# Kernel tuning notes

Hardware: AMD Instinct MI355X
Metric: run time of the kernel (lower is better)

Reference implementation:

```python
import jax, jax.numpy as jnp
import numpy as np

EMBED = 128
HEADS = 16
N = 10000
E = 160000
NEG_SLOPE = 0.2


def setup_inputs() -> dict:
    key = jax.random.key(0)
    ks = jax.random.split(key, 12)
    s = 0.05
    return {
        "x": jax.random.normal(ks[0], (N, EMBED), jnp.float32),
        "edge_index": jax.random.randint(ks[1], (2, E), 0, N, jnp.int64),
        # gat1: in=EMBED, out=EMBED, heads=16, concat
        "W1": jax.random.normal(ks[2], (EMBED, HEADS * EMBED), jnp.float32) * s,
        "a_src1": jax.random.normal(ks[3], (HEADS, EMBED), jnp.float32) * s,
        "a_dst1": jax.random.normal(ks[4], (HEADS, EMBED), jnp.float32) * s,
        "b1": jnp.zeros((HEADS * EMBED,), jnp.float32),
        # gat2: in=HEADS*EMBED, out=EMBED, heads=1, no concat
        "W2": jax.random.normal(ks[5], (HEADS * EMBED, EMBED), jnp.float32) * s,
        "a_src2": jax.random.normal(ks[6], (1, EMBED), jnp.float32) * s,
        "a_dst2": jax.random.normal(ks[7], (1, EMBED), jnp.float32) * s,
        "b2": jnp.zeros((EMBED,), jnp.float32),
        # classifier
        "Wc": jax.random.normal(ks[8], (EMBED, 1), jnp.float32) * s,
        "bc": jnp.zeros((1,), jnp.float32),
    }


def _gat_layer(x, src, dst, W, a_src, a_dst, b, heads, out_ch, n_nodes):
    # node projection: [N, H, C]
    h = (x @ W).reshape(n_nodes, heads, out_ch)
    # per-node attention logits [N, H]
    al_s = jnp.einsum('nhc,hc->nh', h, a_src)
    al_d = jnp.einsum('nhc,hc->nh', h, a_dst)
    # per-edge logits [E, H]
    e = jax.nn.leaky_relu(al_s[src] + al_d[dst], NEG_SLOPE)
    # segment softmax over incoming edges of each dst node
    m = jax.ops.segment_max(e, dst, num_segments=n_nodes)
    ex = jnp.exp(e - m[dst])
    z = jax.ops.segment_sum(ex, dst, num_segments=n_nodes)
    alpha = ex / (z[dst] + 1e-16)
    # weighted scatter-aggregate [N, H, C]
    msg = h[src] * alpha[:, :, None]
    out = jax.ops.segment_sum(msg, dst, num_segments=n_nodes)
    return out.reshape(n_nodes, heads * out_ch) + b


def reference(x, edge_index, W1, a_src1, a_dst1, b1, W2, a_src2, a_dst2, b2, Wc, bc):
    n_nodes = x.shape[0]
    # PyG GATConv default: add self loops
    loop = jnp.arange(n_nodes, dtype=edge_index.dtype)
    src = jnp.concatenate([edge_index[0], loop])
    dst = jnp.concatenate([edge_index[1], loop])
    h = _gat_layer(x, src, dst, W1, a_src1, a_dst1, b1, HEADS, EMBED, n_nodes)
    h = jax.nn.elu(h)
    h = _gat_layer(h, src, dst, W2, a_src2, a_dst2, b2, 1, EMBED, n_nodes)
    return h @ Wc + bc  # [N, 1]
```

## Files before the change

### kernel.cpp

```cpp
#include <hip/hip_runtime.h>
#include <hip/hip_bf16.h>

#define EMBED 128
#define HEADS 16
#define NEG 0.2f

typedef __attribute__((ext_vector_type(8))) short short8;
typedef __attribute__((ext_vector_type(4))) float floatx4;

static __device__ __forceinline__ float leaky(float x) { return x > 0.f ? x : NEG * x; }

static __device__ __forceinline__ short f2bf_bits(float f) {
  __hip_bfloat16 h = __float2bfloat16(f);
  union { __hip_bfloat16 b; short s; } u;
  u.b = h;
  return u.s;
}


__global__ void k_hist(const int* __restrict__ ei, int E, int N, int* __restrict__ deg) {
  int i = blockIdx.x * blockDim.x + threadIdx.x;
  int Et = E + N;
  if (i >= Et) return;
  int d = (i < E) ? ei[E + i] : (i - E);
  atomicAdd(&deg[d], 1);
}

__global__ __launch_bounds__(256) void k_scan1(const int* __restrict__ deg,
                                               int* __restrict__ excl,
                                               int* __restrict__ bsum, int n) {
  __shared__ int s[256];
  int i = blockIdx.x * 256 + threadIdx.x;
  int v = (i < n) ? deg[i] : 0;
  s[threadIdx.x] = v;
  __syncthreads();
  for (int d = 1; d < 256; d <<= 1) {
    int add = ((int)threadIdx.x >= d) ? s[threadIdx.x - d] : 0;
    __syncthreads();
    s[threadIdx.x] += add;
    __syncthreads();
  }
  if (i < n) excl[i] = s[threadIdx.x] - v;
  if (threadIdx.x == 255) bsum[blockIdx.x] = s[255];
}

__global__ void k_scan2(int* __restrict__ bsum, int nb) {
  if (threadIdx.x == 0 && blockIdx.x == 0) {
    int acc = 0;
    for (int i = 0; i < nb; ++i) { int v = bsum[i]; bsum[i] = acc; acc += v; }
  }
}

__global__ __launch_bounds__(256) void k_scan3(const int* __restrict__ deg,
                                               const int* __restrict__ excl,
                                               const int* __restrict__ bsum,
                                               int* __restrict__ row_ptr,
                                               int* __restrict__ cursor, int n) {
  int i = blockIdx.x * 256 + threadIdx.x;
  if (i < n) {
    int r = excl[i] + bsum[blockIdx.x];
    row_ptr[i] = r;
    cursor[i] = r;
    if (i == n - 1) row_ptr[n] = r + deg[i];
  }
}

__global__ void k_scatter(const int* __restrict__ ei, int E, int N,
                          int* __restrict__ cursor, int* __restrict__ csr_src) {
  int i = blockIdx.x * blockDim.x + threadIdx.x;
  int Et = E + N;
  if (i >= Et) return;
  int s = (i < E) ? ei[i] : (i - E);
  int d = (i < E) ? ei[E + i] : (i - E);
  int pos = atomicAdd(&cursor[d], 1);
  csr_src[pos] = s;
}


__global__ __launch_bounds__(256) void k_prepAll(const float* __restrict__ W1,
                                                 const float* __restrict__ a_src1,
                                                 const float* __restrict__ a_dst1,
                                                 const float* __restrict__ W2,
                                                 const float* __restrict__ a_src2,
                                                 const float* __restrict__ a_dst2,
                                                 const float* __restrict__ Wc,
                                                 const float* __restrict__ b2,
                                                 const float* __restrict__ bc,
                                                 float* __restrict__ wsAll,
                                                 float* __restrict__ uvec,
                                                 float* __restrict__ cconst) {
  int gid = blockIdx.x * 256 + threadIdx.x;
  if (gid < 4096) {
    int sel = gid >> 11;
    int id = gid & 2047;
    int h = id >> 7, k = id & 127;
    const float* av = sel ? a_dst1 : a_src1;
    float sum = 0.f;
    const float* wrow = W1 + (size_t)k * 2048 + h * 128;
    const float* arow = av + h * 128;
#pragma unroll 4
    for (int c = 0; c < 128; ++c) sum += wrow[c] * arow[c];
    wsAll[gid] = sum;
  } else if (gid < 10240) {
    int g = gid - 4096;
    int sel = g >> 11;
    int k = g & 2047;
    const float* v = sel == 0 ? Wc : (sel == 1 ? a_src2 : a_dst2);
    const float* wrow = W2 + (size_t)k * 128;
    float s = 0.f;
#pragma unroll 4
    for (int j = 0; j < 128; ++j) s += wrow[j] * v[j];
    uvec[g] = s;
  } else if (gid == 10240) {
    float s = 0.f;
    for (int j = 0; j < 128; ++j) s += b2[j] * Wc[j];
    *cconst = s + bc[0];
  }
}


__global__ __launch_bounds__(256) void k_prep2aT(const float* __restrict__ W1,
                                                 short* __restrict__ hi,
                                                 short* __restrict__ lo) {
  __shared__ float tile[64][65];
  int h = blockIdx.x;
  int c0 = blockIdx.y * 64;
  int j0 = blockIdx.z * 64;
  int t = threadIdx.x;
#pragma unroll
  for (int i = 0; i < 4; ++i) {
    int idx4 = i * 256 + t;
    int c = idx4 >> 4, j4 = idx4 & 15;
    float4 v = *(const float4*)&W1[(size_t)(c0 + c) * 2048 + h * 128 + j0 + j4 * 4];
    tile[c][j4 * 4 + 0] = v.x;
    tile[c][j4 * 4 + 1] = v.y;
    tile[c][j4 * 4 + 2] = v.z;
    tile[c][j4 * 4 + 3] = v.w;
  }
  __syncthreads();
#pragma unroll
  for (int i = 0; i < 4; ++i) {
    int idx = i * 256 + t;
    int j = idx >> 4, c4 = idx & 15;
    unsigned short vh[4], vl[4];
#pragma unroll
    for (int ii = 0; ii < 4; ++ii) {
      float wv = tile[c4 * 4 + ii][j];
      short hb = f2bf_bits(wv);
      float hf = __uint_as_float(((unsigned int)(unsigned short)hb) << 16);
      vh[ii] = (unsigned short)hb;
      vl[ii] = (unsigned short)f2bf_bits(wv - hf);
    }
    size_t o = (size_t)h * 16384 + (size_t)(j0 + j) * 128 + c0 + c4 * 4;
    *(ushort4*)&hi[o] = make_ushort4(vh[0], vh[1], vh[2], vh[3]);
    *(ushort4*)&lo[o] = make_ushort4(vl[0], vl[1], vl[2], vl[3]);
  }
}


__global__ __launch_bounds__(256) void k_al1v2(const float* __restrict__ x,
                                               const float* __restrict__ wsAll,
                                               float* __restrict__ als,
                                               float* __restrict__ ald, int N) {
  __shared__ float wss[128][16], wsd[128][16];
  int tid = threadIdx.x;
  for (int i = tid; i < 2048; i += 256) {
    int h = i >> 7, c = i & 127;
    wss[c][h] = wsAll[i];
    wsd[c][h] = wsAll[2048 + i];
  }
  __syncthreads();
  int gid = blockIdx.x * 256 + tid;
  int n = gid >> 4, h = gid & 15;
  if (n >= N) return;
  const float4* xp = (const float4*)(x + (size_t)n * 128);
  float ps = 0.f, pd = 0.f;
#pragma unroll 8
  for (int c4 = 0; c4 < 32; ++c4) {
    float4 xv = xp[c4];
    int c = c4 * 4;
    ps += xv.x * wss[c][h] + xv.y * wss[c + 1][h] + xv.z * wss[c + 2][h] + xv.w * wss[c + 3][h];
    pd += xv.x * wsd[c][h] + xv.y * wsd[c + 1][h] + xv.z * wsd[c + 2][h] + xv.w * wsd[c + 3][h];
  }
  als[gid] = ps;
  ald[gid] = pd;
}


__global__ __launch_bounds__(256) void k_attn1h(const float* __restrict__ x,
                                                const float* __restrict__ als,
                                                const float* __restrict__ ald,
                                                const int* __restrict__ row_ptr,
                                                const int* __restrict__ csr,
                                                __hip_bfloat16* __restrict__ xaggb,
                                                int N) {
  __shared__ float accsh[2][64][37];

  int tid = threadIdx.x;
  int w = tid >> 6, lane = tid & 63;
  int slot = w >> 1, half = w & 1;
  int d = blockIdx.x * 2 + slot;
  bool active = d < N;

  int e0 = 0, deg = 0;
  if (active) {
    e0 = row_ptr[d];
    deg = row_ptr[d + 1] - e0;
  }

  int g = lane >> 4, c8 = lane & 15;
  float4 aldh4;
  if (active) aldh4 = *(const float4*)&ald[(size_t)d * 16 + g * 4];
  else aldh4 = make_float4(0.f, 0.f, 0.f, 0.f);

  float acc[4][8];
  float zacc[4] = {0.f, 0.f, 0.f, 0.f};
#pragma unroll
  for (int hh = 0; hh < 4; ++hh)
#pragma unroll
    for (int i = 0; i < 8; ++i) acc[hh][i] = 0.f;

  if (active) {
    const float* xc = x + c8 * 8;
    for (int e = half; e < deg; e += 2) {
      int s = csr[e0 + e];
      float4 alv = *(const float4*)&als[(size_t)s * 16 + g * 4];
      const float4* xp = (const float4*)(xc + (size_t)s * 128);
      float4 xa = xp[0], xb = xp[1];
      float ev0 = __expf(leaky(alv.x + aldh4.x));
      float ev1 = __expf(leaky(alv.y + aldh4.y));
      float ev2 = __expf(leaky(alv.z + aldh4.z));
      float ev3 = __expf(leaky(alv.w + aldh4.w));
      zacc[0] += ev0; zacc[1] += ev1; zacc[2] += ev2; zacc[3] += ev3;
      acc[0][0] += ev0 * xa.x; acc[0][1] += ev0 * xa.y; acc[0][2] += ev0 * xa.z; acc[0][3] += ev0 * xa.w;
      acc[0][4] += ev0 * xb.x; acc[0][5] += ev0 * xb.y; acc[0][6] += ev0 * xb.z; acc[0][7] += ev0 * xb.w;
      acc[1][0] += ev1 * xa.x; acc[1][1] += ev1 * xa.y; acc[1][2] += ev1 * xa.z; acc[1][3] += ev1 * xa.w;
      acc[1][4] += ev1 * xb.x; acc[1][5] += ev1 * xb.y; acc[1][6] += ev1 * xb.z; acc[1][7] += ev1 * xb.w;
      acc[2][0] += ev2 * xa.x; acc[2][1] += ev2 * xa.y; acc[2][2] += ev2 * xa.z; acc[2][3] += ev2 * xa.w;
      acc[2][4] += ev2 * xb.x; acc[2][5] += ev2 * xb.y; acc[2][6] += ev2 * xb.z; acc[2][7] += ev2 * xb.w;
      acc[3][0] += ev3 * xa.x; acc[3][1] += ev3 * xa.y; acc[3][2] += ev3 * xa.z; acc[3][3] += ev3 * xa.w;
      acc[3][4] += ev3 * xb.x; acc[3][5] += ev3 * xb.y; acc[3][6] += ev3 * xb.z; acc[3][7] += ev3 * xb.w;
    }
  }

  if (half == 1) {
#pragma unroll
    for (int hh = 0; hh < 4; ++hh) {
#pragma unroll
      for (int i = 0; i < 8; ++i)
        accsh[slot][lane][hh * 8 + i] = acc[hh][i];
      accsh[slot][lane][32 + hh] = zacc[hh];
    }
  }
  __syncthreads();
  if (half == 0 && active) {
#pragma unroll
    for (int hh = 0; hh < 4; ++hh) {
      int h = g * 4 + hh;
      float z = zacc[hh] + accsh[slot][lane][32 + hh];
      float iz = 1.f / (z + 1e-16f);
      __hip_bfloat16 t[8];
#pragma unroll
      for (int i = 0; i < 8; ++i) {
        float v = (acc[hh][i] + accsh[slot][lane][hh * 8 + i]) * iz;
        t[i] = __float2bfloat16(v);
      }
      *(uint4*)(xaggb + (size_t)h * N * 128 + (size_t)d * 128 + c8 * 8) = *(uint4*)t;
    }
  }
}


__global__ __launch_bounds__(256, 2) void k_fused(const __hip_bfloat16* __restrict__ xaggb,
                                                  const short* __restrict__ w1t_hi,
                                                  const short* __restrict__ w1t_lo,
                                                  const float* __restrict__ b1,
                                                  const float* __restrict__ uvec,
                                                  float* __restrict__ partH,
                                                  int N) {
  __shared__ float sh[512];
  __shared__ __align__(16) char Bh[32768];
  __shared__ __align__(16) char Bl[32768];
  int tid = threadIdx.x;
  int h = blockIdx.y;
  int n0 = blockIdx.x * 256;

  for (int i = tid; i < 512; i += 256) {
    int arr = i >> 7, jj = i & 127;
    sh[i] = (arr == 0) ? b1[h * 128 + jj] : uvec[(arr - 1) * 2048 + h * 128 + jj];
  }
  const char* gbh = (const char*)(w1t_hi + (size_t)h * 16384);
  const char* gbl = (const char*)(w1t_lo + (size_t)h * 16384);
#pragma unroll
  for (int i = 0; i < 8; ++i) {
    int ci = i * 256 + tid;
    int row = ci >> 4, kc = ci & 15;
    int po = row * 256 + ((kc ^ (row & 15)) << 4);
    *(uint4*)(Bh + po) = *(const uint4*)(gbh + ci * 16);
    *(uint4*)(Bl + po) = *(const uint4*)(gbl + ci * 16);
  }

  int w = tid >> 6, lane = tid & 63;
  int quad = lane >> 4, l15 = lane & 15;
  int nw = n0 + w * 64;

  const char* abase = (const char*)xaggb + (size_t)h * N * 256;
  short8 a[4][4];
#pragma unroll
  for (int nt = 0; nt < 4; ++nt) {
    int node = nw + nt * 16 + l15;
    if (node >= N) node = N - 1;
    const char* rowp = abase + (size_t)node * 256 + quad * 16;
#pragma unroll
    for (int ks = 0; ks < 4; ++ks)
      a[nt][ks] = *(const short8*)(rowp + ks * 64);
  }
  __syncthreads();

  floatx4 acc[4][8];
#pragma unroll
  for (int jt = 0; jt < 8; ++jt) {
    floatx4 bb = *(const floatx4*)&sh[jt * 16 + quad * 4];
#pragma unroll
    for (int nt = 0; nt < 4; ++nt) acc[nt][jt] = bb;
  }

  for (int ks = 0; ks < 4; ++ks) {
    int xo = (((ks * 4 + quad) ^ l15) << 4);
#pragma unroll
    for (int jt = 0; jt < 8; ++jt) {
      int po = (jt * 16 + l15) * 256 + xo;
      short8 wh = *(const short8*)(Bh + po);
      short8 wl = *(const short8*)(Bl + po);
#pragma unroll
      for (int nt = 0; nt < 4; ++nt) {
        acc[nt][jt] = __builtin_amdgcn_mfma_f32_16x16x32_bf16(wh, a[nt][ks], acc[nt][jt], 0, 0, 0);
        acc[nt][jt] = __builtin_amdgcn_mfma_f32_16x16x32_bf16(wl, a[nt][ks], acc[nt][jt], 0, 0, 0);
      }
    }
  }

  float pc[4] = {0.f, 0.f, 0.f, 0.f};
  float ps[4] = {0.f, 0.f, 0.f, 0.f};
  float pd[4] = {0.f, 0.f, 0.f, 0.f};
#pragma unroll
  for (int jt = 0; jt < 8; ++jt) {
    floatx4 uc = *(const floatx4*)&sh[128 + jt * 16 + quad * 4];
    floatx4 us = *(const floatx4*)&sh[256 + jt * 16 + quad * 4];
    floatx4 ud = *(const floatx4*)&sh[384 + jt * 16 + quad * 4];
#pragma unroll
    for (int nt = 0; nt < 4; ++nt) {
#pragma unroll
      for (int r = 0; r < 4; ++r) {
        float v = acc[nt][jt][r];
        float e = v > 0.f ? v : (__expf(v) - 1.f);
        pc[nt] += e * uc[r];
        ps[nt] += e * us[r];
        pd[nt] += e * ud[r];
      }
    }
  }
  float* pcH = partH + (size_t)h * N;
  float* psH = partH + (size_t)(16 + h) * N;
  float* pdH = partH + (size_t)(32 + h) * N;
#pragma unroll
  for (int nt = 0; nt < 4; ++nt) {
    float c = pc[nt], s = ps[nt], dd = pd[nt];
    c += __shfl_xor(c, 16); c += __shfl_xor(c, 32);
    s += __shfl_xor(s, 16); s += __shfl_xor(s, 32);
    dd += __shfl_xor(dd, 16); dd += __shfl_xor(dd, 32);
    int node = nw + nt * 16 + l15;
    if (quad == 0 && node < N) {
      pcH[node] = c;
      psH[node] = s;
      pdH[node] = dd;
    }
  }
}


__global__ __launch_bounds__(256) void k_redparts(const float* __restrict__ partH,
                                                  float* __restrict__ partc,
                                                  float* __restrict__ parts,
                                                  float* __restrict__ partd, int N) {
  int n = blockIdx.x * 256 + threadIdx.x;
  if (n >= N) return;
  float c = 0.f, s = 0.f, d = 0.f;
#pragma unroll
  for (int h = 0; h < 16; ++h) {
    c += partH[(size_t)h * N + n];
    s += partH[(size_t)(16 + h) * N + n];
    d += partH[(size_t)(32 + h) * N + n];
  }
  partc[n] = c;
  parts[n] = s;
  partd[n] = d;
}


__global__ __launch_bounds__(256) void k_attn2s(const float* __restrict__ partc,
                                                const float* __restrict__ parts,
                                                const float* __restrict__ partd,
                                                const int* __restrict__ row_ptr,
                                                const int* __restrict__ csr,
                                                const float* __restrict__ cconst,
                                                float* __restrict__ out, int N) {
  int w = threadIdx.x >> 6, lane = threadIdx.x & 63;
  int d = blockIdx.x * 4 + w;
  if (d >= N) return;
  int e0 = row_ptr[d], deg = row_ptr[d + 1] - e0;
  float aldd = partd[d];
  float z = 0.f, num = 0.f;
  for (int e = lane; e < deg; e += 64) {
    int s = csr[e0 + e];
    float v = __expf(leaky(parts[s] + aldd));
    z += v;
    num += v * partc[s];
  }
#pragma unroll
  for (int off = 32; off; off >>= 1) {
    z += __shfl_xor(z, off);
    num += __shfl_xor(num, off);
  }
  if (lane == 0) out[d] = num / (z + 1e-16f) + cconst[0];
}


extern "C" void kernel_launch(void* const* d_in, const int* in_sizes, int n_in,
                              void* d_out, int out_size, void* d_ws, size_t ws_size,
                              hipStream_t stream) {
  const float* x      = (const float*)d_in[0];
  const int*   ei     = (const int*)d_in[1];
  const float* W1     = (const float*)d_in[2];
  const float* a_src1 = (const float*)d_in[3];
  const float* a_dst1 = (const float*)d_in[4];
  const float* b1     = (const float*)d_in[5];
  const float* W2     = (const float*)d_in[6];
  const float* a_src2 = (const float*)d_in[7];
  const float* a_dst2 = (const float*)d_in[8];
  const float* b2     = (const float*)d_in[9];
  const float* Wc     = (const float*)d_in[10];
  const float* bc     = (const float*)d_in[11];

  int N = in_sizes[0] / EMBED;
  int E = in_sizes[1] / 2;
  int Et = E + N;
  int nScanB = (N + 255) / 256;

  char* ws = (char*)d_ws;
  size_t off = 0;
  auto alloc = [&](size_t bytes) -> void* {
    void* p = ws + off;
    off += (bytes + 255) & ~(size_t)255;
    return p;
  };
  __hip_bfloat16* xaggb = (__hip_bfloat16*)alloc((size_t)N * 2048 * 2 + 65536);
  short* w1t_hi = (short*)alloc((size_t)262144 * 2);
  short* w1t_lo = (short*)alloc((size_t)262144 * 2);
  float* wsAll  = (float*)alloc(4096 * 4);
  float* uvec   = (float*)alloc(6144 * 4);
  float* cconst = (float*)alloc(256);
  float* als1   = (float*)alloc((size_t)N * 16 * 4);
  float* ald1   = (float*)alloc((size_t)N * 16 * 4);
  float* partH  = (float*)alloc((size_t)48 * N * 4);
  float* part   = (float*)alloc((size_t)3 * N * 4);
  float* partc  = part;
  float* parts  = part + N;
  float* partd  = part + 2 * N;
  int* deg      = (int*)alloc((size_t)N * 4);
  int* excl     = (int*)alloc((size_t)N * 4);
  int* bsum     = (int*)alloc((size_t)(nScanB + 1) * 4);
  int* row_ptr  = (int*)alloc((size_t)(N + 1) * 4);
  int* cursor   = (int*)alloc((size_t)N * 4);
  int* csr      = (int*)alloc((size_t)Et * 4);

  hipMemsetAsync(deg, 0, (size_t)N * 4, stream);

  k_hist<<<(Et + 255) / 256, 256, 0, stream>>>(ei, E, N, deg);
  k_scan1<<<nScanB, 256, 0, stream>>>(deg, excl, bsum, N);
  k_scan2<<<1, 64, 0, stream>>>(bsum, nScanB);
  k_scan3<<<nScanB, 256, 0, stream>>>(deg, excl, bsum, row_ptr, cursor, N);
  k_scatter<<<(Et + 255) / 256, 256, 0, stream>>>(ei, E, N, cursor, csr);

  k_prepAll<<<41, 256, 0, stream>>>(W1, a_src1, a_dst1, W2, a_src2, a_dst2, Wc, b2, bc,
                                    wsAll, uvec, cconst);
  k_prep2aT<<<dim3(16, 2, 2), 256, 0, stream>>>(W1, w1t_hi, w1t_lo);

  k_al1v2<<<(N * 16 + 255) / 256, 256, 0, stream>>>(x, wsAll, als1, ald1, N);
  k_attn1h<<<(N + 1) / 2, 256, 0, stream>>>(x, als1, ald1, row_ptr, csr, xaggb, N);

  k_fused<<<dim3((N + 255) / 256, 16), 256, 0, stream>>>(xaggb, w1t_hi, w1t_lo, b1, uvec,
                                                         partH, N);
  k_redparts<<<(N + 255) / 256, 256, 0, stream>>>(partH, partc, parts, partd, N);
  k_attn2s<<<(N + 3) / 4, 256, 0, stream>>>(partc, parts, partd, row_ptr, csr, cconst,
                                            (float*)d_out, N);
}
```

Measured before the change: 189.9 us.

## Merge prep kernels, single-block scan, atomic head reduction, prefetch attention gathers

Folds the two weight-prep kernels and the buffer zeroing into one launch, and replaces the three-kernel scan with a single-block wave-shuffle scan. The separate per-head reduction kernel is removed: the fused GEMM kernel now accumulates its per-head partials straight into the final vectors with float atomics. The layer-1 attention loop caches CSR indices in registers and software-prefetches the next edge's gathers. Layer-2 attention uses 16 lanes per node instead of 64. The aim is fewer launches and better latency hiding, at the cost of atomic contention and summation order that is no longer deterministic.

New measurement: 183.5 us. 3.4% less time.

```diff
diff --git a/kernel.cpp b/kernel.cpp
--- a/kernel.cpp
+++ b/kernel.cpp
@@ -26,43 +26,40 @@
   atomicAdd(&deg[d], 1);
 }
 
-__global__ __launch_bounds__(256) void k_scan1(const int* __restrict__ deg,
-                                               int* __restrict__ excl,
-                                               int* __restrict__ bsum, int n) {
-  __shared__ int s[256];
-  int i = blockIdx.x * 256 + threadIdx.x;
-  int v = (i < n) ? deg[i] : 0;
-  s[threadIdx.x] = v;
-  __syncthreads();
-  for (int d = 1; d < 256; d <<= 1) {
-    int add = ((int)threadIdx.x >= d) ? s[threadIdx.x - d] : 0;
+__global__ __launch_bounds__(1024) void k_scan(const int* __restrict__ deg,
+                                               int* __restrict__ row_ptr,
+                                               int* __restrict__ cursor, int N) {
+  __shared__ int wsum[16];
+  int tid = threadIdx.x;
+  int lane = tid & 63, w = tid >> 6;
+  int base = 0;
+  for (int c0 = 0; c0 < N; c0 += 1024) {
+    int i = c0 + tid;
+    int v = (i < N) ? deg[i] : 0;
+    int s = v;
+#pragma unroll
+    for (int dd = 1; dd < 64; dd <<= 1) {
+      int t = __shfl_up(s, dd);
+      if (lane >= dd) s += t;
+    }
+    if (lane == 63) wsum[w] = s;
     __syncthreads();
-    s[threadIdx.x] += add;
+    int carry = 0, ctot = 0;
+#pragma unroll
+    for (int k = 0; k < 16; ++k) {
+      int t = wsum[k];
+      ctot += t;
+      if (k < w) carry += t;
+    }
+    int excl = base + carry + s - v;
+    if (i < N) {
+      row_ptr[i] = excl;
+      cursor[i] = excl;
+    }
+    base += ctot;
     __syncthreads();
   }
-  if (i < n) excl[i] = s[threadIdx.x] - v;
-  if (threadIdx.x == 255) bsum[blockIdx.x] = s[255];
-}
-
-__global__ void k_scan2(int* __restrict__ bsum, int nb) {
-  if (threadIdx.x == 0 && blockIdx.x == 0) {
-    int acc = 0;
-    for (int i = 0; i < nb; ++i) { int v = bsum[i]; bsum[i] = acc; acc += v; }
-  }
-}
-
-__global__ __launch_bounds__(256) void k_scan3(const int* __restrict__ deg,
-                                               const int* __restrict__ excl,
-                                               const int* __restrict__ bsum,
-                                               int* __restrict__ row_ptr,
-                                               int* __restrict__ cursor, int n) {
-  int i = blockIdx.x * 256 + threadIdx.x;
-  if (i < n) {
-    int r = excl[i] + bsum[blockIdx.x];
-    row_ptr[i] = r;
-    cursor[i] = r;
-    if (i == n - 1) row_ptr[n] = r + deg[i];
-  }
+  if (tid == 0) row_ptr[N] = base;
 }
 
 __global__ void k_scatter(const int* __restrict__ ei, int E, int N,
@@ -77,19 +74,61 @@
 }
 
 
-__global__ __launch_bounds__(256) void k_prepAll(const float* __restrict__ W1,
-                                                 const float* __restrict__ a_src1,
-                                                 const float* __restrict__ a_dst1,
-                                                 const float* __restrict__ W2,
-                                                 const float* __restrict__ a_src2,
-                                                 const float* __restrict__ a_dst2,
-                                                 const float* __restrict__ Wc,
-                                                 const float* __restrict__ b2,
-                                                 const float* __restrict__ bc,
-                                                 float* __restrict__ wsAll,
-                                                 float* __restrict__ uvec,
-                                                 float* __restrict__ cconst) {
-  int gid = blockIdx.x * 256 + threadIdx.x;
+__global__ __launch_bounds__(256) void k_prep(const float* __restrict__ W1,
+                                              const float* __restrict__ a_src1,
+                                              const float* __restrict__ a_dst1,
+                                              const float* __restrict__ W2,
+                                              const float* __restrict__ a_src2,
+                                              const float* __restrict__ a_dst2,
+                                              const float* __restrict__ Wc,
+                                              const float* __restrict__ b2,
+                                              const float* __restrict__ bc,
+                                              float* __restrict__ wsAll,
+                                              float* __restrict__ uvec,
+                                              float* __restrict__ cconst,
+                                              short* __restrict__ hi,
+                                              short* __restrict__ lo,
+                                              float* __restrict__ part,
+                                              int* __restrict__ deg,
+                                              int N) {
+  __shared__ float tile[64][65];
+  if (blockIdx.x < 64) {
+    int b = blockIdx.x;
+    int h = b & 15;
+    int c0 = ((b >> 4) & 1) * 64;
+    int j0 = ((b >> 5) & 1) * 64;
+    int t = threadIdx.x;
+#pragma unroll
+    for (int i = 0; i < 4; ++i) {
+      int idx4 = i * 256 + t;
+      int c = idx4 >> 4, j4 = idx4 & 15;
+      float4 v = *(const float4*)&W1[(size_t)(c0 + c) * 2048 + h * 128 + j0 + j4 * 4];
+      tile[c][j4 * 4 + 0] = v.x;
+      tile[c][j4 * 4 + 1] = v.y;
+      tile[c][j4 * 4 + 2] = v.z;
+      tile[c][j4 * 4 + 3] = v.w;
+    }
+    __syncthreads();
+#pragma unroll
+    for (int i = 0; i < 4; ++i) {
+      int idx = i * 256 + t;
+      int j = idx >> 4, c4 = idx & 15;
+      unsigned short vh[4], vl[4];
+#pragma unroll
+      for (int ii = 0; ii < 4; ++ii) {
+        float wv = tile[c4 * 4 + ii][j];
+        short hb = f2bf_bits(wv);
+        float hf = __uint_as_float(((unsigned int)(unsigned short)hb) << 16);
+        vh[ii] = (unsigned short)hb;
+        vl[ii] = (unsigned short)f2bf_bits(wv - hf);
+      }
+      size_t o = (size_t)h * 16384 + (size_t)(j0 + j) * 128 + c0 + c4 * 4;
+      *(ushort4*)&hi[o] = make_ushort4(vh[0], vh[1], vh[2], vh[3]);
+      *(ushort4*)&lo[o] = make_ushort4(vl[0], vl[1], vl[2], vl[3]);
+    }
+    return;
+  }
+  int gid = (blockIdx.x - 64) * 256 + threadIdx.x;
   if (gid < 4096) {
     int sel = gid >> 11;
     int id = gid & 2047;
@@ -115,45 +154,10 @@
     float s = 0.f;
     for (int j = 0; j < 128; ++j) s += b2[j] * Wc[j];
     *cconst = s + bc[0];
-  }
-}
-
-
-__global__ __launch_bounds__(256) void k_prep2aT(const float* __restrict__ W1,
-                                                 short* __restrict__ hi,
-                                                 short* __restrict__ lo) {
-  __shared__ float tile[64][65];
-  int h = blockIdx.x;
-  int c0 = blockIdx.y * 64;
-  int j0 = blockIdx.z * 64;
-  int t = threadIdx.x;
-#pragma unroll
-  for (int i = 0; i < 4; ++i) {
-    int idx4 = i * 256 + t;
-    int c = idx4 >> 4, j4 = idx4 & 15;
-    float4 v = *(const float4*)&W1[(size_t)(c0 + c) * 2048 + h * 128 + j0 + j4 * 4];
-    tile[c][j4 * 4 + 0] = v.x;
-    tile[c][j4 * 4 + 1] = v.y;
-    tile[c][j4 * 4 + 2] = v.z;
-    tile[c][j4 * 4 + 3] = v.w;
-  }
-  __syncthreads();
-#pragma unroll
-  for (int i = 0; i < 4; ++i) {
-    int idx = i * 256 + t;
-    int j = idx >> 4, c4 = idx & 15;
-    unsigned short vh[4], vl[4];
-#pragma unroll
-    for (int ii = 0; ii < 4; ++ii) {
-      float wv = tile[c4 * 4 + ii][j];
-      short hb = f2bf_bits(wv);
-      float hf = __uint_as_float(((unsigned int)(unsigned short)hb) << 16);
-      vh[ii] = (unsigned short)hb;
-      vl[ii] = (unsigned short)f2bf_bits(wv - hf);
-    }
-    size_t o = (size_t)h * 16384 + (size_t)(j0 + j) * 128 + c0 + c4 * 4;
-    *(ushort4*)&hi[o] = make_ushort4(vh[0], vh[1], vh[2], vh[3]);
-    *(ushort4*)&lo[o] = make_ushort4(vl[0], vl[1], vl[2], vl[3]);
+  } else if (gid >= 10496) {
+    int z = gid - 10496;
+    if (z < 3 * N) part[z] = 0.f;
+    else if (z < 4 * N) deg[z - 3 * N] = 0;
   }
 }
 
@@ -209,9 +213,8 @@
   }
 
   int g = lane >> 4, c8 = lane & 15;
-  float4 aldh4;
+  float4 aldh4 = make_float4(0.f, 0.f, 0.f, 0.f);
   if (active) aldh4 = *(const float4*)&ald[(size_t)d * 16 + g * 4];
-  else aldh4 = make_float4(0.f, 0.f, 0.f, 0.f);
 
   float acc[4][8];
   float zacc[4] = {0.f, 0.f, 0.f, 0.f};
@@ -221,25 +224,53 @@
     for (int i = 0; i < 8; ++i) acc[hh][i] = 0.f;
 
   if (active) {
+    int sreg = 0;
+    if (lane < deg) sreg = csr[e0 + lane];
     const float* xc = x + c8 * 8;
-    for (int e = half; e < deg; e += 2) {
-      int s = csr[e0 + e];
-      float4 alv = *(const float4*)&als[(size_t)s * 16 + g * 4];
-      const float4* xp = (const float4*)(xc + (size_t)s * 128);
-      float4 xa = xp[0], xb = xp[1];
-      float ev0 = __expf(leaky(alv.x + aldh4.x));
-      float ev1 = __expf(leaky(alv.y + aldh4.y));
-      float ev2 = __expf(leaky(alv.z + aldh4.z));
-      float ev3 = __expf(leaky(alv.w + aldh4.w));
+
+    int e = half;
+    bool have = e < deg;
+    int sC = 0;
+    float4 alC = make_float4(0.f, 0.f, 0.f, 0.f);
+    float4 xaC = alC, xbC = alC;
+    if (have) {
+      sC = (e < 64) ? __shfl(sreg, e) : csr[e0 + e];
+      alC = *(const float4*)&als[(size_t)sC * 16 + g * 4];
+      const float4* xp = (const float4*)(xc + (size_t)sC * 128);
+      xaC = xp[0];
+      xbC = xp[1];
+    }
+    while (have) {
+      int e2 = e + 2;
+      bool have2 = e2 < deg;
+      int sN = 0;
+      float4 alN = alC, xaN = xaC, xbN = xbC;
+      if (have2) {
+        sN = (e2 < 64) ? __shfl(sreg, e2) : csr[e0 + e2];
+        alN = *(const float4*)&als[(size_t)sN * 16 + g * 4];
+        const float4* xp2 = (const float4*)(xc + (size_t)sN * 128);
+        xaN = xp2[0];
+        xbN = xp2[1];
+      }
+      float ev0 = __expf(leaky(alC.x + aldh4.x));
+      float ev1 = __expf(leaky(alC.y + aldh4.y));
+      float ev2 = __expf(leaky(alC.z + aldh4.z));
+      float ev3 = __expf(leaky(alC.w + aldh4.w));
       zacc[0] += ev0; zacc[1] += ev1; zacc[2] += ev2; zacc[3] += ev3;
-      acc[0][0] += ev0 * xa.x; acc[0][1] += ev0 * xa.y; acc[0][2] += ev0 * xa.z; acc[0][3] += ev0 * xa.w;
-      acc[0][4] += ev0 * xb.x; acc[0][5] += ev0 * xb.y; acc[0][6] += ev0 * xb.z; acc[0][7] += ev0 * xb.w;
-      acc[1][0] += ev1 * xa.x; acc[1][1] += ev1 * xa.y; acc[1][2] += ev1 * xa.z; acc[1][3] += ev1 * xa.w;
-      acc[1][4] += ev1 * xb.x; acc[1][5] += ev1 * xb.y; acc[1][6] += ev1 * xb.z; acc[1][7] += ev1 * xb.w;
-      acc[2][0] += ev2 * xa.x; acc[2][1] += ev2 * xa.y; acc[2][2] += ev2 * xa.z; acc[2][3] += ev2 * xa.w;
-      acc[2][4] += ev2 * xb.x; acc[2][5] += ev2 * xb.y; acc[2][6] += ev2 * xb.z; acc[2][7] += ev2 * xb.w;
-      acc[3][0] += ev3 * xa.x; acc[3][1] += ev3 * xa.y; acc[3][2] += ev3 * xa.z; acc[3][3] += ev3 * xa.w;
-      acc[3][4] += ev3 * xb.x; acc[3][5] += ev3 * xb.y; acc[3][6] += ev3 * xb.z; acc[3][7] += ev3 * xb.w;
+      acc[0][0] += ev0 * xaC.x; acc[0][1] += ev0 * xaC.y; acc[0][2] += ev0 * xaC.z; acc[0][3] += ev0 * xaC.w;
+      acc[0][4] += ev0 * xbC.x; acc[0][5] += ev0 * xbC.y; acc[0][6] += ev0 * xbC.z; acc[0][7] += ev0 * xbC.w;
+      acc[1][0] += ev1 * xaC.x; acc[1][1] += ev1 * xaC.y; acc[1][2] += ev1 * xaC.z; acc[1][3] += ev1 * xaC.w;
+      acc[1][4] += ev1 * xbC.x; acc[1][5] += ev1 * xbC.y; acc[1][6] += ev1 * xbC.z; acc[1][7] += ev1 * xbC.w;
+      acc[2][0] += ev2 * xaC.x; acc[2][1] += ev2 * xaC.y; acc[2][2] += ev2 * xaC.z; acc[2][3] += ev2 * xaC.w;
+      acc[2][4] += ev2 * xbC.x; acc[2][5] += ev2 * xbC.y; acc[2][6] += ev2 * xbC.z; acc[2][7] += ev2 * xbC.w;
+      acc[3][0] += ev3 * xaC.x; acc[3][1] += ev3 * xaC.y; acc[3][2] += ev3 * xaC.z; acc[3][3] += ev3 * xaC.w;
+      acc[3][4] += ev3 * xbC.x; acc[3][5] += ev3 * xbC.y; acc[3][6] += ev3 * xbC.z; acc[3][7] += ev3 * xbC.w;
+      e = e2;
+      have = have2;
+      sC = sN;
+      alC = alN;
+      xaC = xaN;
+      xbC = xbN;
     }
   }
 
@@ -276,7 +307,9 @@
                                                   const short* __restrict__ w1t_lo,
                                                   const float* __restrict__ b1,
                                                   const float* __restrict__ uvec,
-                                                  float* __restrict__ partH,
+                                                  float* __restrict__ partc,
+                                                  float* __restrict__ parts,
+                                                  float* __restrict__ partd,
                                                   int N) {
   __shared__ float sh[512];
   __shared__ __align__(16) char Bh[32768];
@@ -360,9 +393,6 @@
       }
     }
   }
-  float* pcH = partH + (size_t)h * N;
-  float* psH = partH + (size_t)(16 + h) * N;
-  float* pdH = partH + (size_t)(32 + h) * N;
 #pragma unroll
   for (int nt = 0; nt < 4; ++nt) {
     float c = pc[nt], s = ps[nt], dd = pd[nt];
@@ -371,30 +401,11 @@
     dd += __shfl_xor(dd, 16); dd += __shfl_xor(dd, 32);
     int node = nw + nt * 16 + l15;
     if (quad == 0 && node < N) {
-      pcH[node] = c;
-      psH[node] = s;
-      pdH[node] = dd;
-    }
-  }
-}
-
-
-__global__ __launch_bounds__(256) void k_redparts(const float* __restrict__ partH,
-                                                  float* __restrict__ partc,
-                                                  float* __restrict__ parts,
-                                                  float* __restrict__ partd, int N) {
-  int n = blockIdx.x * 256 + threadIdx.x;
-  if (n >= N) return;
-  float c = 0.f, s = 0.f, d = 0.f;
-#pragma unroll
-  for (int h = 0; h < 16; ++h) {
-    c += partH[(size_t)h * N + n];
-    s += partH[(size_t)(16 + h) * N + n];
-    d += partH[(size_t)(32 + h) * N + n];
-  }
-  partc[n] = c;
-  parts[n] = s;
-  partd[n] = d;
+      atomicAdd(&partc[node], c);
+      atomicAdd(&parts[node], s);
+      atomicAdd(&partd[node], dd);
+    }
+  }
 }
 
 
@@ -405,24 +416,24 @@
                                                 const int* __restrict__ csr,
                                                 const float* __restrict__ cconst,
                                                 float* __restrict__ out, int N) {
-  int w = threadIdx.x >> 6, lane = threadIdx.x & 63;
-  int d = blockIdx.x * 4 + w;
+  int grp = threadIdx.x >> 4, l = threadIdx.x & 15;
+  int d = blockIdx.x * 16 + grp;
   if (d >= N) return;
   int e0 = row_ptr[d], deg = row_ptr[d + 1] - e0;
   float aldd = partd[d];
   float z = 0.f, num = 0.f;
-  for (int e = lane; e < deg; e += 64) {
+  for (int e = l; e < deg; e += 16) {
     int s = csr[e0 + e];
     float v = __expf(leaky(parts[s] + aldd));
     z += v;
     num += v * partc[s];
   }
 #pragma unroll
-  for (int off = 32; off; off >>= 1) {
+  for (int off = 8; off; off >>= 1) {
     z += __shfl_xor(z, off);
     num += __shfl_xor(num, off);
   }
-  if (lane == 0) out[d] = num / (z + 1e-16f) + cconst[0];
+  if (l == 0) out[d] = num / (z + 1e-16f) + cconst[0];
 }
 
 
@@ -445,7 +456,6 @@
   int N = in_sizes[0] / EMBED;
   int E = in_sizes[1] / 2;
   int Et = E + N;
-  int nScanB = (N + 255) / 256;
 
   char* ws = (char*)d_ws;
   size_t off = 0;
@@ -462,36 +472,25 @@
   float* cconst = (float*)alloc(256);
   float* als1   = (float*)alloc((size_t)N * 16 * 4);
   float* ald1   = (float*)alloc((size_t)N * 16 * 4);
-  float* partH  = (float*)alloc((size_t)48 * N * 4);
   float* part   = (float*)alloc((size_t)3 * N * 4);
   float* partc  = part;
   float* parts  = part + N;
   float* partd  = part + 2 * N;
   int* deg      = (int*)alloc((size_t)N * 4);
-  int* excl     = (int*)alloc((size_t)N * 4);
-  int* bsum     = (int*)alloc((size_t)(nScanB + 1) * 4);
   int* row_ptr  = (int*)alloc((size_t)(N + 1) * 4);
   int* cursor   = (int*)alloc((size_t)N * 4);
   int* csr      = (int*)alloc((size_t)Et * 4);
 
-  hipMemsetAsync(deg, 0, (size_t)N * 4, stream);
-
+  int nPrepB = 64 + (10496 + 4 * N + 255) / 256;
+  k_prep<<<nPrepB, 256, 0, stream>>>(W1, a_src1, a_dst1, W2, a_src2, a_dst2, Wc, b2, bc,
+                                     wsAll, uvec, cconst, w1t_hi, w1t_lo, part, deg, N);
   k_hist<<<(Et + 255) / 256, 256, 0, stream>>>(ei, E, N, deg);
-  k_scan1<<<nScanB, 256, 0, stream>>>(deg, excl, bsum, N);
-  k_scan2<<<1, 64, 0, stream>>>(bsum, nScanB);
-  k_scan3<<<nScanB, 256, 0, stream>>>(deg, excl, bsum, row_ptr, cursor, N);
+  k_scan<<<1, 1024, 0, stream>>>(deg, row_ptr, cursor, N);
   k_scatter<<<(Et + 255) / 256, 256, 0, stream>>>(ei, E, N, cursor, csr);
-
-  k_prepAll<<<41, 256, 0, stream>>>(W1, a_src1, a_dst1, W2, a_src2, a_dst2, Wc, b2, bc,
-                                    wsAll, uvec, cconst);
-  k_prep2aT<<<dim3(16, 2, 2), 256, 0, stream>>>(W1, w1t_hi, w1t_lo);
-
   k_al1v2<<<(N * 16 + 255) / 256, 256, 0, stream>>>(x, wsAll, als1, ald1, N);
   k_attn1h<<<(N + 1) / 2, 256, 0, stream>>>(x, als1, ald1, row_ptr, csr, xaggb, N);
-
   k_fused<<<dim3((N + 255) / 256, 16), 256, 0, stream>>>(xaggb, w1t_hi, w1t_lo, b1, uvec,
-                                                         partH, N);
-  k_redparts<<<(N + 255) / 256, 256, 0, stream>>>(partH, partc, parts, partd, N);
-  k_attn2s<<<(N + 3) / 4, 256, 0, stream>>>(partc, parts, partd, row_ptr, csr, cconst,
-                                            (float*)d_out, N);
-}
+                                                         partc, parts, partd, N);
+  k_attn2s<<<(N + 15) / 16, 256, 0, stream>>>(partc, parts, partd, row_ptr, csr, cconst,
+                                              (float*)d_out, N);
+}
```
